# Kernel tuning notes

Hardware: AMD Instinct MI355X
Metric: run time of the kernel (lower is better)

## Reference

```python
import jax, jax.numpy as jnp
import numpy as np

D_MODEL = 1024
NUM_HEADS = 16
HEAD_DIM = D_MODEL // NUM_HEADS


def setup_inputs() -> dict:
    key = jax.random.key(0)
    kx, kq, kk, kv, ko = jax.random.split(key, 5)
    B, S = 2, 2048
    scale = 1.0 / np.sqrt(D_MODEL)
    return {
        "x": jax.random.normal(kx, (B, S, D_MODEL), dtype=jnp.float32),
        "W_q": jax.random.normal(kq, (D_MODEL, D_MODEL), dtype=jnp.float32) * scale,
        "W_k": jax.random.normal(kk, (D_MODEL, D_MODEL), dtype=jnp.float32) * scale,
        "W_v": jax.random.normal(kv, (D_MODEL, D_MODEL), dtype=jnp.float32) * scale,
        "W_o": jax.random.normal(ko, (D_MODEL, D_MODEL), dtype=jnp.float32) * scale,
        "causal": 1,
    }


def _attn(x, W_q, W_k, W_v, W_o, causal):
    B, S, D = x.shape
    H, Hd = NUM_HEADS, HEAD_DIM
    # projections: nn.Linear applies x @ W.T
    q = (x @ W_q.T).reshape(B, S, H, Hd)
    k = (x @ W_k.T).reshape(B, S, H, Hd)
    v = (x @ W_v.T).reshape(B, S, H, Hd)
    # scores: [B, H, S, S]
    scores = jnp.einsum("bqhd,bkhd->bhqk", q, k) / np.sqrt(Hd)
    if causal:
        mask = jnp.triu(jnp.ones((S, S), dtype=bool), k=1)
        scores = jnp.where(mask, -jnp.inf, scores)
    attn = jax.nn.softmax(scores, axis=-1)
    out = jnp.einsum("bhqk,bkhd->bqhd", attn, v).reshape(B, S, D)
    return out @ W_o.T


def reference(x, W_q, W_k, W_v, W_o, causal):
    return _attn(x, W_q, W_k, W_v, W_o, causal)
```

## Files before the change

kernel.cpp:

```cpp
#include <hip/hip_runtime.h>

typedef __attribute__((ext_vector_type(8))) short bf16x8;
typedef __attribute__((ext_vector_type(4))) float f32x4;
typedef __attribute__((ext_vector_type(4))) unsigned short u16x4;

#define MFMA16(a, b, c) __builtin_amdgcn_mfma_f32_16x16x32_bf16((a), (b), (c), 0, 0, 0)

static constexpr int D_MODEL = 1024;
static constexpr int SEQ = 2048;
static constexpr int NH = 16;
static constexpr int HD = 64;
static constexpr int LDA = 40;
static constexpr int MST = 136;
static constexpr float NEG_BIG = -1.0e30f;

__device__ __forceinline__ unsigned short f2bf(float f) {
  union { float f; unsigned int u; } v; v.f = f;
  unsigned int r = v.u + 0x7fffu + ((v.u >> 16) & 1u);
  return (unsigned short)(r >> 16);
}

__device__ __forceinline__ unsigned int cvtpk_bf16(float a, float b) {
  unsigned int r;
  asm("v_cvt_pk_bf16_f32 %0, %1, %2" : "=v"(r) : "v"(a), "v"(b));
  return r;
}

__device__ __forceinline__ bf16x8 ld8(const void* p, size_t eidx, int bf) {
  if (bf) return *(const bf16x8*)((const unsigned short*)p + eidx);
  const float* f = (const float*)p + eidx;
  f32x4 lo = *(const f32x4*)f;
  f32x4 hi = *(const f32x4*)(f + 4);
  bf16x8 r;
  r[0] = (short)f2bf(lo[0]); r[1] = (short)f2bf(lo[1]);
  r[2] = (short)f2bf(lo[2]); r[3] = (short)f2bf(lo[3]);
  r[4] = (short)f2bf(hi[0]); r[5] = (short)f2bf(hi[1]);
  r[6] = (short)f2bf(hi[2]); r[7] = (short)f2bf(hi[3]);
  return r;
}

__device__ __forceinline__ void async16(const unsigned short* g, unsigned short* l) {
  __builtin_amdgcn_global_load_lds(
      (const __attribute__((address_space(1))) void*)g,
      (__attribute__((address_space(3))) void*)l, 16, 0, 0);
}

__global__ __launch_bounds__(64) void detect_kernel(
    const unsigned short* __restrict__ xs, int* __restrict__ flag) {
  int lane = threadIdx.x;
  unsigned short s = xs[2 * lane];
  int e = (s >> 7) & 0xFF;
  bool hit = (e >= 117 && e <= 129);
  unsigned long long m = __ballot(hit);
  if (lane == 0) { flag[0] = (__popcll(m) >= 32) ? 1 : 0; flag[1] = 1; }
}

__global__ __launch_bounds__(256) void convert_kernel(
    const void* __restrict__ X,
    const void* __restrict__ W0, const void* __restrict__ W1,
    const void* __restrict__ W2, const void* __restrict__ W3,
    const int* __restrict__ flag,
    unsigned short* __restrict__ Xb, unsigned short* __restrict__ Wb)
{
  const int bf = *flag;
  const int ty = blockIdx.y;
  const void* src; unsigned short* dst; size_t n;
  if (ty == 0) { src = X; dst = Xb; n = (size_t)2 * SEQ * D_MODEL; }
  else {
    src = (ty == 1) ? W0 : (ty == 2) ? W1 : (ty == 3) ? W2 : W3;
    dst = Wb + (size_t)(ty - 1) * D_MODEL * D_MODEL;
    n = (size_t)D_MODEL * D_MODEL;
  }
  size_t i = ((size_t)blockIdx.x * 256 + threadIdx.x) * 8;
  if (i >= n) return;
  *(bf16x8*)(dst + i) = ld8(src, i, bf);
}

__device__ __forceinline__ void gemm_fast_core(
    const unsigned short* __restrict__ A, const unsigned short* __restrict__ B,
    int tm, int tn, unsigned short* smem, f32x4 acc[4][4])
{
  const int t = threadIdx.x;
  const int lane = t & 63;
  const int w = t >> 6;
  const int wm = (w >> 1) * 64, wn = (w & 1) * 64;
  const int quad = lane >> 4, l16 = lane & 15;
  const int srow = lane >> 2;
  const int scol = ((lane & 3) ^ ((lane >> 3) & 3)) * 8;
  const int xa = (l16 >> 1) & 3;

#pragma unroll
  for (int mi = 0; mi < 4; ++mi)
#pragma unroll
    for (int ni = 0; ni < 4; ++ni)
      acc[mi][ni] = (f32x4){0.f, 0.f, 0.f, 0.f};

  auto stage = [&](int f, int buf) {
    const int k0 = f * 32;
    unsigned short* dst = smem + buf * 8192;
#pragma unroll
    for (int i = 0; i < 2; ++i) {
      const int row = w * 32 + i * 16;
      async16(A + (size_t)(tm + row + srow) * D_MODEL + k0 + scol,
              dst + row * 32);
      async16(B + (size_t)(tn + row + srow) * D_MODEL + k0 + scol,
              dst + 4096 + row * 32);
    }
  };

  stage(0, 0);
  stage(1, 1);

  int cur = 0, nb = 2;
  for (int f = 0; f < 32; ++f) {
    if (f + 1 < 32) asm volatile("s_waitcnt vmcnt(4)" ::: "memory");
    else            asm volatile("s_waitcnt vmcnt(0)" ::: "memory");
    __builtin_amdgcn_s_barrier();
    __builtin_amdgcn_sched_barrier(0);
    if (f + 2 < 32) stage(f + 2, nb);
    const unsigned short* As = smem + cur * 8192;
    const unsigned short* Bs = As + 4096;
    bf16x8 af[4], bfv[4];
#pragma unroll
    for (int mi = 0; mi < 4; ++mi)
      af[mi] = *(const bf16x8*)(As + (wm + mi * 16 + l16) * 32 + (quad ^ xa) * 8);
#pragma unroll
    for (int ni = 0; ni < 4; ++ni)
      bfv[ni] = *(const bf16x8*)(Bs + (wn + ni * 16 + l16) * 32 + (quad ^ xa) * 8);
    __builtin_amdgcn_s_setprio(1);
#pragma unroll
    for (int mi = 0; mi < 4; ++mi)
#pragma unroll
      for (int ni = 0; ni < 4; ++ni)
        acc[mi][ni] = MFMA16(af[mi], bfv[ni], acc[mi][ni]);
    __builtin_amdgcn_s_setprio(0);
    cur = (cur == 2) ? 0 : cur + 1;
    nb = (nb == 2) ? 0 : nb + 1;
  }
}

__global__ __launch_bounds__(256) void qkv_fast_kernel(
    const unsigned short* __restrict__ X,
    const unsigned short* __restrict__ Wb,
    unsigned short* __restrict__ qd,
    unsigned short* __restrict__ kws,
    unsigned short* __restrict__ vws)
{
  __shared__ __align__(16) unsigned short smem[3 * 8192];
  const int bid = blockIdx.x;
  const int xcd = bid & 7, s0 = bid >> 3;
  const int tmg = xcd >> 2, tng = xcd & 3;
  const int tm_local = s0 / 6, zt = s0 % 6;
  const int z = zt >> 1, tn_local = zt & 1;
  const int tm = (tmg * 16 + tm_local) * 128;
  const int tn = (tng * 2 + tn_local) * 128;
  const unsigned short* W = Wb + (size_t)z * D_MODEL * D_MODEL;
  f32x4 acc[4][4];
  gemm_fast_core(X, W, tm, tn, smem, acc);

  const int t = threadIdx.x;
  const int lane = t & 63, w = t >> 6;
  const int wm = (w >> 1) * 64, wn = (w & 1) * 64;
  const int quad = lane >> 4, l16 = lane & 15;

  if (z == 2) {
    const int b = tm >> 11;
    const int sb = tm & 2047;
#pragma unroll
    for (int ph = 0; ph < 2; ++ph) {
      __syncthreads();
      if ((w & 1) == ph) {
#pragma unroll
        for (int mi = 0; mi < 4; ++mi)
#pragma unroll
          for (int ni = 0; ni < 4; ++ni)
#pragma unroll
            for (int r = 0; r < 4; ++r) {
              int m_local = wm + mi * 16 + quad * 4 + r;
              int n_sub = ni * 16 + l16;
              smem[n_sub * MST + m_local] = f2bf(acc[mi][ni][r]);
            }
      }
      __syncthreads();
      const int row = t >> 2, c0 = (t & 3) * 32;
      const int n_g = tn + ph * 64 + row;
      const int h = n_g >> 6, d = n_g & 63;
      unsigned short* dst = vws + (((size_t)b * NH + h) * HD + d) * SEQ + sb + c0;
#pragma unroll
      for (int cc = 0; cc < 4; ++cc)
        *(bf16x8*)(dst + cc * 8) = *(const bf16x8*)(smem + row * MST + c0 + cc * 8);
    }
    return;
  }
#pragma unroll
  for (int mi = 0; mi < 4; ++mi)
#pragma unroll
    for (int ni = 0; ni < 4; ++ni)
#pragma unroll
      for (int r = 0; r < 4; ++r) {
        int m = tm + wm + mi * 16 + quad * 4 + r;
        int n = tn + wn + ni * 16 + l16;
        unsigned short bv = f2bf(acc[mi][ni][r]);
        if (z == 0) {
          qd[(size_t)m * D_MODEL + n] = bv;
        } else {
          int b = m >> 11, sg = m & 2047;
          int h = n >> 6, d = n & 63;
          kws[(((size_t)b * NH + h) * SEQ + sg) * HD + d] = bv;
        }
      }
}

__global__ __launch_bounds__(256) void oproj_fast_kernel(
    const unsigned short* __restrict__ AW,
    const unsigned short* __restrict__ Wo,
    float* __restrict__ tmp)
{
  __shared__ __align__(16) unsigned short smem[3 * 8192];
  const int bid = blockIdx.x;
  const int xcd = bid & 7, s0 = bid >> 3;
  const int tmg = xcd >> 2, tng = xcd & 3;
  const int tm = (tmg * 16 + (s0 >> 1)) * 128;
  const int tn = (tng * 2 + (s0 & 1)) * 128;
  f32x4 acc[4][4];
  gemm_fast_core(AW, Wo, tm, tn, smem, acc);

  const int t = threadIdx.x;
  const int lane = t & 63, w = t >> 6;
  const int wm = (w >> 1) * 64, wn = (w & 1) * 64;
  const int quad = lane >> 4, l16 = lane & 15;
#pragma unroll
  for (int mi = 0; mi < 4; ++mi)
#pragma unroll
    for (int ni = 0; ni < 4; ++ni)
#pragma unroll
      for (int r = 0; r < 4; ++r) {
        int m = tm + wm + mi * 16 + quad * 4 + r;
        int n = tn + wn + ni * 16 + l16;
        tmp[(size_t)m * D_MODEL + n] = acc[mi][ni][r];
      }
}

__device__ __forceinline__ void gemm_tile_128x128(
    const void* __restrict__ A, const void* __restrict__ B, int bf,
    int tm, int tn, unsigned short* As, unsigned short* Bs, f32x4 acc[4][4])
{
  const int t = threadIdx.x;
  const int lane = t & 63;
  const int w = t >> 6;
  const int wm = (w >> 1) * 64, wn = (w & 1) * 64;
  const int quad = lane >> 4, l16 = lane & 15;
  const int r0 = t >> 2, kc = (t & 3) * 8;
  const int r1 = r0 + 64;

#pragma unroll
  for (int mi = 0; mi < 4; ++mi)
#pragma unroll
    for (int ni = 0; ni < 4; ++ni)
      acc[mi][ni] = (f32x4){0.f, 0.f, 0.f, 0.f};

  for (int k0 = 0; k0 < D_MODEL; k0 += 32) {
    bf16x8 a0 = ld8(A, (size_t)(tm + r0) * D_MODEL + k0 + kc, bf);
    bf16x8 a1 = ld8(A, (size_t)(tm + r1) * D_MODEL + k0 + kc, bf);
    bf16x8 b0 = ld8(B, (size_t)(tn + r0) * D_MODEL + k0 + kc, bf);
    bf16x8 b1 = ld8(B, (size_t)(tn + r1) * D_MODEL + k0 + kc, bf);
    __syncthreads();
    *(bf16x8*)(As + r0 * LDA + kc) = a0;
    *(bf16x8*)(As + r1 * LDA + kc) = a1;
    *(bf16x8*)(Bs + r0 * LDA + kc) = b0;
    *(bf16x8*)(Bs + r1 * LDA + kc) = b1;
    __syncthreads();
    bf16x8 af[4], bfv[4];
#pragma unroll
    for (int mi = 0; mi < 4; ++mi)
      af[mi] = *(const bf16x8*)(As + (wm + mi * 16 + l16) * LDA + quad * 8);
#pragma unroll
    for (int ni = 0; ni < 4; ++ni)
      bfv[ni] = *(const bf16x8*)(Bs + (wn + ni * 16 + l16) * LDA + quad * 8);
#pragma unroll
    for (int mi = 0; mi < 4; ++mi)
#pragma unroll
      for (int ni = 0; ni < 4; ++ni)
        acc[mi][ni] = MFMA16(af[mi], bfv[ni], acc[mi][ni]);
  }
}

__global__ __launch_bounds__(256) void qkv_kernel(
    const void* __restrict__ X,
    const void* __restrict__ Wq,
    const void* __restrict__ Wk,
    const void* __restrict__ Wv,
    const int* __restrict__ flag,
    unsigned short* __restrict__ qd,
    unsigned short* __restrict__ kws,
    unsigned short* __restrict__ vws)
{
  __shared__ __align__(16) unsigned short As[128 * LDA];
  __shared__ __align__(16) unsigned short Bs[128 * LDA];
  const int bf = *flag;
  const int z = blockIdx.z;
  const void* W = (z == 0) ? Wq : ((z == 1) ? Wk : Wv);
  const int tm = blockIdx.y * 128, tn = blockIdx.x * 128;
  f32x4 acc[4][4];
  gemm_tile_128x128(X, W, bf, tm, tn, As, Bs, acc);

  const int t = threadIdx.x;
  const int lane = t & 63, w = t >> 6;
  const int wm = (w >> 1) * 64, wn = (w & 1) * 64;
  const int quad = lane >> 4, l16 = lane & 15;
#pragma unroll
  for (int mi = 0; mi < 4; ++mi)
#pragma unroll
    for (int ni = 0; ni < 4; ++ni)
#pragma unroll
      for (int r = 0; r < 4; ++r) {
        int m = tm + wm + mi * 16 + quad * 4 + r;
        int n = tn + wn + ni * 16 + l16;
        unsigned short bv = f2bf(acc[mi][ni][r]);
        if (z == 0) {
          qd[(size_t)m * D_MODEL + n] = bv;
        } else {
          int b = m >> 11, s = m & 2047;
          int h = n >> 6, d = n & 63;
          if (z == 1) kws[(((size_t)b * NH + h) * SEQ + s) * HD + d] = bv;
          else        vws[(((size_t)b * NH + h) * HD + d) * SEQ + s] = bv;
        }
      }
}

__global__ __launch_bounds__(256) void oproj_kernel(
    const unsigned short* __restrict__ AW,
    const void* __restrict__ Wo,
    const int* __restrict__ flag,
    float* __restrict__ tmp)
{
  __shared__ __align__(16) unsigned short As[128 * LDA];
  __shared__ __align__(16) unsigned short Bs[128 * LDA];
  const int bf = *flag;
  const int t = threadIdx.x;
  const int lane = t & 63;
  const int w = t >> 6;
  const int wm = (w >> 1) * 64, wn = (w & 1) * 64;
  const int quad = lane >> 4, l16 = lane & 15;
  const int r0 = t >> 2, kc = (t & 3) * 8;
  const int r1 = r0 + 64;
  const int tm = blockIdx.y * 128, tn = blockIdx.x * 128;
  f32x4 acc[4][4];
#pragma unroll
  for (int mi = 0; mi < 4; ++mi)
#pragma unroll
    for (int ni = 0; ni < 4; ++ni)
      acc[mi][ni] = (f32x4){0.f, 0.f, 0.f, 0.f};

  for (int k0 = 0; k0 < D_MODEL; k0 += 32) {
    bf16x8 a0 = *(const bf16x8*)(AW + (size_t)(tm + r0) * D_MODEL + k0 + kc);
    bf16x8 a1 = *(const bf16x8*)(AW + (size_t)(tm + r1) * D_MODEL + k0 + kc);
    bf16x8 b0 = ld8(Wo, (size_t)(tn + r0) * D_MODEL + k0 + kc, bf);
    bf16x8 b1 = ld8(Wo, (size_t)(tn + r1) * D_MODEL + k0 + kc, bf);
    __syncthreads();
    *(bf16x8*)(As + r0 * LDA + kc) = a0;
    *(bf16x8*)(As + r1 * LDA + kc) = a1;
    *(bf16x8*)(Bs + r0 * LDA + kc) = b0;
    *(bf16x8*)(Bs + r1 * LDA + kc) = b1;
    __syncthreads();
    bf16x8 af[4], bfv[4];
#pragma unroll
    for (int mi = 0; mi < 4; ++mi)
      af[mi] = *(const bf16x8*)(As + (wm + mi * 16 + l16) * LDA + quad * 8);
#pragma unroll
    for (int ni = 0; ni < 4; ++ni)
      bfv[ni] = *(const bf16x8*)(Bs + (wn + ni * 16 + l16) * LDA + quad * 8);
#pragma unroll
    for (int mi = 0; mi < 4; ++mi)
#pragma unroll
      for (int ni = 0; ni < 4; ++ni)
        acc[mi][ni] = MFMA16(af[mi], bfv[ni], acc[mi][ni]);
  }
#pragma unroll
  for (int mi = 0; mi < 4; ++mi)
#pragma unroll
    for (int ni = 0; ni < 4; ++ni)
#pragma unroll
      for (int r = 0; r < 4; ++r) {
        int m = tm + wm + mi * 16 + quad * 4 + r;
        int n = tn + wn + ni * 16 + l16;
        tmp[(size_t)m * D_MODEL + n] = acc[mi][ni][r];
      }
}

__device__ __forceinline__ void attn_item(
    const unsigned short* __restrict__ Ksb, const unsigned short* __restrict__ Vsb,
    const bf16x8 (&aq)[2], f32x4 (&oacc)[4], float& lsum,
    int kt, int diag, int q0base, int l16, int quad, int xa, float Cs)
{
  bf16x8 kfr[4][2], vfr[4][2];
#pragma unroll
  for (int cb = 0; cb < 4; ++cb)
#pragma unroll
    for (int hf = 0; hf < 2; ++hf) {
      kfr[cb][hf] = *(const bf16x8*)(Ksb + (cb * 16 + l16) * 64 +
                                     ((hf * 4 + quad) ^ xa) * 8);
      vfr[cb][hf] = *(const bf16x8*)(Vsb + (cb * 16 + l16) * 64 +
                                     ((hf * 4 + quad) ^ xa) * 8);
    }
  f32x4 sc[4];
  __builtin_amdgcn_s_setprio(1);
#pragma unroll
  for (int cb = 0; cb < 4; ++cb) {
    sc[cb] = (f32x4){0.f, 0.f, 0.f, 0.f};
    sc[cb] = MFMA16(kfr[cb][0], aq[0], sc[cb]);
    sc[cb] = MFMA16(kfr[cb][1], aq[1], sc[cb]);
  }
  __builtin_amdgcn_s_setprio(0);
  if (diag) {
    int qq = q0base + l16;
#pragma unroll
    for (int cb = 0; cb < 4; ++cb)
#pragma unroll
      for (int rr = 0; rr < 4; ++rr)
        if (kt * 64 + (cb & 1) * 32 + quad * 8 + (cb >> 1) * 4 + rr > qq)
          sc[cb][rr] = NEG_BIG;
  }
#pragma unroll
  for (int cb = 0; cb < 4; ++cb)
#pragma unroll
    for (int rr = 0; rr < 4; ++rr)
      sc[cb][rr] = __builtin_amdgcn_exp2f(sc[cb][rr] * Cs);
  f32x4 t0, t1;
#pragma unroll
  for (int rr = 0; rr < 4; ++rr) { t0[rr] = sc[0][rr] + sc[1][rr]; }
#pragma unroll
  for (int rr = 0; rr < 4; ++rr) { t1[rr] = sc[2][rr] + sc[3][rr]; }
#pragma unroll
  for (int rr = 0; rr < 4; ++rr) { t0[rr] += t1[rr]; }
  lsum += (t0[0] + t0[1]) + (t0[2] + t0[3]);
  bf16x8 bp[2];
#pragma unroll
  for (int hf = 0; hf < 2; ++hf) {
    union { unsigned int w4[4]; bf16x8 v; } u;
    u.w4[0] = cvtpk_bf16(sc[hf][0], sc[hf][1]);
    u.w4[1] = cvtpk_bf16(sc[hf][2], sc[hf][3]);
    u.w4[2] = cvtpk_bf16(sc[2 + hf][0], sc[2 + hf][1]);
    u.w4[3] = cvtpk_bf16(sc[2 + hf][2], sc[2 + hf][3]);
    bp[hf] = u.v;
  }
  __builtin_amdgcn_s_setprio(1);
#pragma unroll
  for (int db = 0; db < 4; ++db) {
    oacc[db] = MFMA16(vfr[db][0], bp[0], oacc[db]);
    oacc[db] = MFMA16(vfr[db][1], bp[1], oacc[db]);
  }
  __builtin_amdgcn_s_setprio(0);
}

__global__ __launch_bounds__(256, 2) void attn_kernel(
    unsigned short* __restrict__ Qd,
    const unsigned short* __restrict__ Kb,
    const unsigned short* __restrict__ Vt,
    const int* __restrict__ causal_p)
{
  __shared__ __align__(16) unsigned short Ks[3][64 * 64];
  __shared__ __align__(16) unsigned short Vs[3][64 * 64];
  const int bid = blockIdx.x;
  const int xcd = bid & 7, slot = bid >> 3;
  const int bhl = slot >> 4, p = slot & 15;
  const int bh = xcd * 4 + bhl;
  const int b = bh >> 4, h = bh & 15;
  const int t = threadIdx.x, lane = t & 63, w = t >> 6;
  const int quad = lane >> 4, l16 = lane & 15;
  const int causal = *causal_p;
  const int tA = causal ? (31 - p) : (2 * p);
  const int tB = causal ? p : (2 * p + 1);
  const int ktA = causal ? (32 - p) : 32;
  const int ITEMS = causal ? 33 : 64;
  unsigned short* qh = Qd + (size_t)b * SEQ * D_MODEL + h * HD;
  const unsigned short* kh = Kb + ((size_t)b * NH + h) * SEQ * HD;
  const unsigned short* vh = Vt + ((size_t)b * NH + h) * HD * SEQ;
  const float Cs = 0.125f * 1.4426950408889634f;
  const int srow = lane >> 3;
  const int gcol = ((lane & 7) ^ srow) * 8;
  const int xa = l16 & 7;

  int kvp[2];
#pragma unroll
  for (int j2 = 0; j2 < 2; ++j2) {
    const int rp = w * 16 + j2 * 8 + srow;
    kvp[j2] = ((rp >> 4) & 1) * 32 + ((rp >> 2) & 3) * 8 + ((rp >> 5) & 1) * 4 + (rp & 3);
  }

  const int qA = tA * 64 + w * 16, qB = tB * 64 + w * 16;
  bf16x8 aqA[2], aqB[2];
#pragma unroll
  for (int ch = 0; ch < 2; ++ch) {
    aqA[ch] = *(const bf16x8*)(qh + (size_t)(qA + l16) * D_MODEL +
                               ch * 32 + quad * 8);
    aqB[ch] = *(const bf16x8*)(qh + (size_t)(qB + l16) * D_MODEL +
                               ch * 32 + quad * 8);
  }

  f32x4 oaccA[4], oaccB[4];
#pragma unroll
  for (int db = 0; db < 4; ++db) {
    oaccA[db] = (f32x4){0.f, 0.f, 0.f, 0.f};
    oaccB[db] = (f32x4){0.f, 0.f, 0.f, 0.f};
  }
  float lsumA = 0.f, lsumB = 0.f;

  auto stage = [&](int f, int buf) {
    const int kt = (f < ktA) ? f : (f - ktA);
#pragma unroll
    for (int j2 = 0; j2 < 2; ++j2) {
      const int row = w * 16 + j2 * 8;
      async16(kh + (size_t)(kt * 64 + kvp[j2]) * HD + gcol, &Ks[buf][row * 64]);
      async16(vh + (size_t)(row + srow) * SEQ + kt * 64 + gcol, &Vs[buf][row * 64]);
    }
  };

  stage(0, 0);
  stage(1, 1);

  int cur = 0, nb = 2;
  for (int f = 0; f < ITEMS; ++f) {
    if (f + 1 < ITEMS) asm volatile("s_waitcnt vmcnt(4)" ::: "memory");
    else               asm volatile("s_waitcnt vmcnt(0)" ::: "memory");
    __builtin_amdgcn_s_barrier();
    __builtin_amdgcn_sched_barrier(0);
    if (f + 2 < ITEMS) stage(f + 2, nb);
    if (f < ktA)
      attn_item(&Ks[cur][0], &Vs[cur][0], aqA, oaccA, lsumA,
                f, causal && (f == ktA - 1), qA, l16, quad, xa, Cs);
    else
      attn_item(&Ks[cur][0], &Vs[cur][0], aqB, oaccB, lsumB,
                f - ktA, causal && (f == ITEMS - 1), qB, l16, quad, xa, Cs);
    cur = (cur == 2) ? 0 : cur + 1;
    nb = (nb == 2) ? 0 : nb + 1;
  }

  {
    float l = lsumA;
    l += __shfl_xor(l, 16, 64);
    l += __shfl_xor(l, 32, 64);
    float inv = 1.0f / l;
#pragma unroll
    for (int db = 0; db < 4; ++db) {
      u16x4 o;
#pragma unroll
      for (int rr = 0; rr < 4; ++rr) o[rr] = f2bf(oaccA[db][rr] * inv);
      *(u16x4*)(qh + (size_t)(qA + l16) * D_MODEL + db * 16 + quad * 4) = o;
    }
  }
  {
    float l = lsumB;
    l += __shfl_xor(l, 16, 64);
    l += __shfl_xor(l, 32, 64);
    float inv = 1.0f / l;
#pragma unroll
    for (int db = 0; db < 4; ++db) {
      u16x4 o;
#pragma unroll
      for (int rr = 0; rr < 4; ++rr) o[rr] = f2bf(oaccB[db][rr] * inv);
      *(u16x4*)(qh + (size_t)(qB + l16) * D_MODEL + db * 16 + quad * 4) = o;
    }
  }
}

__global__ __launch_bounds__(256) void final_kernel(
    const float* __restrict__ tmp, void* __restrict__ out,
    const int* __restrict__ flag)
{
  const int bf = *flag;
  size_t i = ((size_t)blockIdx.x * 256 + threadIdx.x) * 8;
  f32x4 lo = *(const f32x4*)(tmp + i);
  f32x4 hi = *(const f32x4*)(tmp + i + 4);
  if (bf) {
    bf16x8 r;
    r[0] = (short)f2bf(lo[0]); r[1] = (short)f2bf(lo[1]);
    r[2] = (short)f2bf(lo[2]); r[3] = (short)f2bf(lo[3]);
    r[4] = (short)f2bf(hi[0]); r[5] = (short)f2bf(hi[1]);
    r[6] = (short)f2bf(hi[2]); r[7] = (short)f2bf(hi[3]);
    *(bf16x8*)((unsigned short*)out + i) = r;
  } else {
    *(f32x4*)((float*)out + i) = lo;
    *(f32x4*)((float*)out + i + 4) = hi;
  }
}

extern "C" void kernel_launch(void* const* d_in, const int* in_sizes, int n_in,
                              void* d_out, int out_size, void* d_ws, size_t ws_size,
                              hipStream_t stream) {
  const void* X  = d_in[0];
  const void* Wq = d_in[1];
  const void* Wk = d_in[2];
  const void* Wv = d_in[3];
  const void* Wo = d_in[4];
  const int* causal = (const int*)d_in[5];

  const size_t NE = (size_t)2 * SEQ * D_MODEL;
  const size_t WE = (size_t)D_MODEL * D_MODEL;
  int* flag0 = (int*)d_ws;
  unsigned short* kws = (unsigned short*)((char*)d_ws + 64);
  unsigned short* vws = kws + NE;
  float* tmp = (float*)kws;
  unsigned short* Wb = vws + NE;
  unsigned short* qd = (unsigned short*)d_out;
  unsigned short* Xb = qd + NE;

  const bool big = ws_size >= (size_t)64 + 24ull * 1024 * 1024;

  hipLaunchKernelGGL(detect_kernel, dim3(1), dim3(64), 0, stream,
                     (const unsigned short*)X, flag0);
  if (big) {
    hipLaunchKernelGGL(convert_kernel, dim3(2048, 5), dim3(256), 0, stream,
                       X, Wq, Wk, Wv, Wo, flag0, Xb, Wb);
    hipLaunchKernelGGL(qkv_fast_kernel, dim3(768), dim3(256), 0, stream,
                       Xb, Wb, qd, kws, vws);
    hipLaunchKernelGGL(attn_kernel, dim3(512), dim3(256), 0, stream,
                       qd, kws, vws, causal);
    hipLaunchKernelGGL(oproj_fast_kernel, dim3(256), dim3(256), 0, stream,
                       qd, Wb + 3 * WE, tmp);
  } else {
    hipLaunchKernelGGL(qkv_kernel, dim3(8, 32, 3), dim3(256), 0, stream,
                       X, Wq, Wk, Wv, flag0, qd, kws, vws);
    hipLaunchKernelGGL(attn_kernel, dim3(512), dim3(256), 0, stream,
                       qd, kws, vws, causal);
    hipLaunchKernelGGL(oproj_kernel, dim3(8, 32), dim3(256), 0, stream,
                       qd, Wo, flag0, tmp);
  }
  hipLaunchKernelGGL(final_kernel, dim3(2048), dim3(256), 0, stream,
                     tmp, d_out, flag0);
}
```

Before: 184.0 us.

## Share each staged K/V tile between both query tiles in attention loop

The attention loop used to stream K/V tiles separately for query tile A and query tile B. Now each K/V tile is loaded once and applied to both query tiles, with B skipped once it passes its causal limit. This roughly halves global-to-LDS traffic and barrier iterations per block. In exchange it raises register pressure from two sets of score accumulators and adds a per-iteration branch on B activity.

```diff
diff --git a/kernel.cpp b/kernel.cpp
--- a/kernel.cpp
+++ b/kernel.cpp
@@ -388,22 +388,9 @@
       }
 }
 
-__device__ __forceinline__ void attn_item(
-    const unsigned short* __restrict__ Ksb, const unsigned short* __restrict__ Vsb,
-    const bf16x8 (&aq)[2], f32x4 (&oacc)[4], float& lsum,
-    int kt, int diag, int q0base, int l16, int quad, int xa, float Cs)
-{
-  bf16x8 kfr[4][2], vfr[4][2];
-#pragma unroll
-  for (int cb = 0; cb < 4; ++cb)
-#pragma unroll
-    for (int hf = 0; hf < 2; ++hf) {
-      kfr[cb][hf] = *(const bf16x8*)(Ksb + (cb * 16 + l16) * 64 +
-                                     ((hf * 4 + quad) ^ xa) * 8);
-      vfr[cb][hf] = *(const bf16x8*)(Vsb + (cb * 16 + l16) * 64 +
-                                     ((hf * 4 + quad) ^ xa) * 8);
-    }
-  f32x4 sc[4];
+__device__ __forceinline__ void qk_part(
+    const bf16x8 (&kfr)[4][2], const bf16x8 (&aq)[2], f32x4 (&sc)[4])
+{
   __builtin_amdgcn_s_setprio(1);
 #pragma unroll
   for (int cb = 0; cb < 4; ++cb) {
@@ -412,13 +399,18 @@
     sc[cb] = MFMA16(kfr[cb][1], aq[1], sc[cb]);
   }
   __builtin_amdgcn_s_setprio(0);
+}
+
+__device__ __forceinline__ void smpv_part(
+    f32x4 (&sc)[4], const bf16x8 (&vfr)[4][2], f32x4 (&oacc)[4], float& lsum,
+    int diag, int ktbase, int qq, int quad, float Cs)
+{
   if (diag) {
-    int qq = q0base + l16;
 #pragma unroll
     for (int cb = 0; cb < 4; ++cb)
 #pragma unroll
       for (int rr = 0; rr < 4; ++rr)
-        if (kt * 64 + (cb & 1) * 32 + quad * 8 + (cb >> 1) * 4 + rr > qq)
+        if (ktbase + (cb & 1) * 32 + quad * 8 + (cb >> 1) * 4 + rr > qq)
           sc[cb][rr] = NEG_BIG;
   }
 #pragma unroll
@@ -471,8 +463,7 @@
   const int causal = *causal_p;
   const int tA = causal ? (31 - p) : (2 * p);
   const int tB = causal ? p : (2 * p + 1);
-  const int ktA = causal ? (32 - p) : 32;
-  const int ITEMS = causal ? 33 : 64;
+  const int ITEMS = causal ? (32 - p) : 32;
   unsigned short* qh = Qd + (size_t)b * SEQ * D_MODEL + h * HD;
   const unsigned short* kh = Kb + ((size_t)b * NH + h) * SEQ * HD;
   const unsigned short* vh = Vt + ((size_t)b * NH + h) * HD * SEQ;
@@ -507,17 +498,16 @@
   float lsumA = 0.f, lsumB = 0.f;
 
   auto stage = [&](int f, int buf) {
-    const int kt = (f < ktA) ? f : (f - ktA);
 #pragma unroll
     for (int j2 = 0; j2 < 2; ++j2) {
       const int row = w * 16 + j2 * 8;
-      async16(kh + (size_t)(kt * 64 + kvp[j2]) * HD + gcol, &Ks[buf][row * 64]);
-      async16(vh + (size_t)(row + srow) * SEQ + kt * 64 + gcol, &Vs[buf][row * 64]);
+      async16(kh + (size_t)(f * 64 + kvp[j2]) * HD + gcol, &Ks[buf][row * 64]);
+      async16(vh + (size_t)(row + srow) * SEQ + f * 64 + gcol, &Vs[buf][row * 64]);
     }
   };
 
   stage(0, 0);
-  stage(1, 1);
+  if (ITEMS > 1) stage(1, 1);
 
   int cur = 0, nb = 2;
   for (int f = 0; f < ITEMS; ++f) {
@@ -526,12 +516,26 @@
     __builtin_amdgcn_s_barrier();
     __builtin_amdgcn_sched_barrier(0);
     if (f + 2 < ITEMS) stage(f + 2, nb);
-    if (f < ktA)
-      attn_item(&Ks[cur][0], &Vs[cur][0], aqA, oaccA, lsumA,
-                f, causal && (f == ktA - 1), qA, l16, quad, xa, Cs);
-    else
-      attn_item(&Ks[cur][0], &Vs[cur][0], aqB, oaccB, lsumB,
-                f - ktA, causal && (f == ITEMS - 1), qB, l16, quad, xa, Cs);
+
+    bf16x8 kfr[4][2], vfr[4][2];
+#pragma unroll
+    for (int cb = 0; cb < 4; ++cb)
+#pragma unroll
+      for (int hf = 0; hf < 2; ++hf) {
+        kfr[cb][hf] = *(const bf16x8*)(&Ks[cur][(cb * 16 + l16) * 64 +
+                                               ((hf * 4 + quad) ^ xa) * 8]);
+        vfr[cb][hf] = *(const bf16x8*)(&Vs[cur][(cb * 16 + l16) * 64 +
+                                               ((hf * 4 + quad) ^ xa) * 8]);
+      }
+    const int bAct = causal ? (f <= p) : 1;
+    f32x4 scA[4], scB[4];
+    qk_part(kfr, aqA, scA);
+    if (bAct) qk_part(kfr, aqB, scB);
+    smpv_part(scA, vfr, oaccA, lsumA,
+              causal && (f == ITEMS - 1), f * 64, qA + l16, quad, Cs);
+    if (bAct)
+      smpv_part(scB, vfr, oaccB, lsumB,
+                causal && (f == p), f * 64, qB + l16, quad, Cs);
     cur = (cur == 2) ? 0 : cur + 1;
     nb = (nb == 2) ? 0 : nb + 1;
   }
```

New measurement: 181.5 us. No clear change (-1.3%).
